# Performance work log

Hardware: AMD Instinct MI355X
Metric: run time of the kernel (lower is better)

## Reference

```python
import jax, jax.numpy as jnp
import numpy as np

OUT_SL = 32


def gru_cell(x, h, Wih, Whh, bih, bhh):
    # PyTorch GRU cell: gates ordered (r, z, n)
    gi = x @ Wih.T + bih
    gh = h @ Whh.T + bhh
    ir, iz, inn = jnp.split(gi, 3, axis=-1)
    hr, hz, hn = jnp.split(gh, 3, axis=-1)
    r = jax.nn.sigmoid(ir + hr)
    z = jax.nn.sigmoid(iz + hz)
    n = jnp.tanh(inn + r * hn)
    return (1.0 - z) * n + z * h


def run_gru_layer(xs, h0, Wih, Whh, bih, bhh, reverse=False):
    def step(h, x):
        h = gru_cell(x, h, Wih, Whh, bih, bhh)
        return h, h
    hT, ys = jax.lax.scan(step, h0, xs, reverse=reverse)
    return ys, hT


def setup_inputs() -> dict:
    key = jax.random.key(0)
    ks = iter(jax.random.split(key, 32))

    def p(shape, fan_in):
        return (jax.random.normal(next(ks), shape, dtype=jnp.float32)
                / np.sqrt(fan_in).astype(np.float32))

    V_ENC, V_DEC, EE, ED, NH = 32000, 32000, 300, 300, 256
    inp = jax.random.randint(next(ks), (128, 64), 0, V_ENC)
    return {
        'emb_enc': p((V_ENC, EE), 1.0),
        'enc_Wih0': p((2, 3 * NH, EE), EE),
        'enc_Whh0': p((2, 3 * NH, NH), NH),
        'enc_bih0': p((2, 3 * NH), NH),
        'enc_bhh0': p((2, 3 * NH), NH),
        'enc_Wih1': p((2, 3 * NH, 2 * NH), 2 * NH),
        'enc_Whh1': p((2, 3 * NH, NH), NH),
        'enc_bih1': p((2, 3 * NH), NH),
        'enc_bhh1': p((2, 3 * NH), NH),
        'W_out_enc': p((ED, 2 * NH), 2 * NH),
        'emb_dec': p((V_DEC, ED), 1.0),
        'dec_Wih': p((2, 3 * ED, ED), ED),
        'dec_Whh': p((2, 3 * ED, ED), ED),
        'dec_bih': p((2, 3 * ED), ED),
        'dec_bhh': p((2, 3 * ED), ED),
        'W1': p((2 * NH, ED), 2 * NH),
        'l2_W': p((ED, ED), ED),
        'l2_b': p((ED,), ED),
        'l3_W': p((ED, ED + 2 * NH), ED + 2 * NH),
        'l3_b': p((ED,), ED),
        'V_att': p((ED,), ED),
        'out_b': p((V_DEC,), ED),
        'inp': inp,
    }


def reference(emb_enc, enc_Wih0, enc_Whh0, enc_bih0, enc_bhh0,
              enc_Wih1, enc_Whh1, enc_bih1, enc_bhh1, W_out_enc,
              emb_dec, dec_Wih, dec_Whh, dec_bih, dec_bhh,
              W1, l2_W, l2_b, l3_W, l3_b, V_att, out_b, inp):
    sl, bs = inp.shape
    nh = enc_Whh0.shape[-1]
    h0 = jnp.zeros((bs, nh), dtype=emb_enc.dtype)

    # ---- encoder: 2-layer bidirectional GRU (dropout in eval mode = identity)
    emb = emb_enc[inp]                                        # (sl, bs, EE)
    yf0, hf0 = run_gru_layer(emb, h0, enc_Wih0[0], enc_Whh0[0], enc_bih0[0], enc_bhh0[0])
    yb0, hb0 = run_gru_layer(emb, h0, enc_Wih0[1], enc_Whh0[1], enc_bih0[1], enc_bhh0[1], reverse=True)
    x1 = jnp.concatenate([yf0, yb0], axis=-1)                 # (sl, bs, 2*nh)
    yf1, hf1 = run_gru_layer(x1, h0, enc_Wih1[0], enc_Whh1[0], enc_bih1[0], enc_bhh1[0])
    yb1, hb1 = run_gru_layer(x1, h0, enc_Wih1[1], enc_Whh1[1], enc_bih1[1], enc_bhh1[1], reverse=True)
    enc_out = jnp.concatenate([yf1, yb1], axis=-1)            # (sl, bs, 2*nh)

    # h.view(2,2,bs,-1).permute(0,2,1,3) -> concat fwd/bwd per layer
    h = jnp.stack([jnp.concatenate([hf0, hb0], axis=-1),
                   jnp.concatenate([hf1, hb1], axis=-1)])     # (2, bs, 2*nh)
    h = h @ W_out_enc.T                                       # (2, bs, ED)

    w1e = enc_out @ W1                                        # (sl, bs, ED)
    dec_inp0 = jnp.zeros((bs,), dtype=jnp.int32)

    def dec_step(carry, _):
        h, dec_inp = carry
        w2h = h[-1] @ l2_W.T + l2_b                           # (bs, ED)
        u = jnp.tanh(w1e + w2h[None])                         # (sl, bs, ED)
        a = jax.nn.softmax(u @ V_att, axis=0)                 # (sl, bs), softmax over seq
        Xa = jnp.einsum('sb,sbd->bd', a, enc_out)             # (bs, 2*nh)
        e = emb_dec[dec_inp]                                  # (bs, ED)
        x = jnp.concatenate([e, Xa], axis=1) @ l3_W.T + l3_b  # (bs, ED)
        h0n = gru_cell(x, h[0], dec_Wih[0], dec_Whh[0], dec_bih[0], dec_bhh[0])
        h1n = gru_cell(h0n, h[1], dec_Wih[1], dec_Whh[1], dec_bih[1], dec_bhh[1])
        outp = h1n @ emb_dec.T + out_b                        # (bs, V_dec), tied weights
        ndec = jnp.argmax(outp, axis=1).astype(jnp.int32)
        return (jnp.stack([h0n, h1n]), ndec), outp

    (_, _), res = jax.lax.scan(dec_step, (h, dec_inp0), None, length=OUT_SL)
    return res                                                # (out_sl, bs, V_dec)
```

## Files before the change

kernel.cpp:

```cpp
#include <hip/hip_runtime.h>
#include <math.h>


typedef unsigned long long ull;
typedef float v2f __attribute__((ext_vector_type(2)));

#define DINL static __device__ __forceinline__

DINL float sigm(float x) { return 1.0f / (1.0f + expf(-x)); }
DINL float dot4f(float4 a, float4 b) { return a.x*b.x + a.y*b.y + a.z*b.z + a.w*b.w; }

DINL ull packmax(float x, int v) {
  unsigned u = __float_as_uint(x);
  u = (u & 0x80000000u) ? ~u : (u | 0x80000000u);
  return ((ull)u << 32) | (unsigned)(~v);
}
DINL ull umax64(ull a, ull b) { return a > b ? a : b; }

DINL float atl(const float* p) {
  unsigned u = __hip_atomic_load((const unsigned*)p, __ATOMIC_RELAXED,
                                 __HIP_MEMORY_SCOPE_AGENT);
  return __uint_as_float(u);
}
DINL void atsf(float* p, float v) {
  __hip_atomic_exchange((unsigned*)p, __float_as_uint(v), __ATOMIC_RELAXED,
                        __HIP_MEMORY_SCOPE_AGENT);
}
DINL ull atl64(const ull* p) {
  return __hip_atomic_load(p, __ATOMIC_RELAXED, __HIP_MEMORY_SCOPE_AGENT);
}
DINL void ats64(ull* p, ull v) {
  __hip_atomic_exchange(p, v, __ATOMIC_RELAXED, __HIP_MEMORY_SCOPE_AGENT);
}

DINL void gbar(unsigned* flags, int wg, unsigned target, int tid) {
  asm volatile("s_waitcnt vmcnt(0)" ::: "memory");
  __syncthreads();
  if (tid == 0)
    __hip_atomic_exchange(&flags[wg * 32], target, __ATOMIC_RELAXED,
                          __HIP_MEMORY_SCOPE_AGENT);
  while (__hip_atomic_load(&flags[tid * 32], __ATOMIC_RELAXED,
                           __HIP_MEMORY_SCOPE_AGENT) < target)
    __builtin_amdgcn_s_sleep(1);
  __syncthreads();
}

__global__ __launch_bounds__(256) void k_embed(const float4* __restrict__ E,
                                               const int* __restrict__ inp,
                                               float4* __restrict__ out) {
  int i = blockIdx.x * 256 + threadIdx.x;
  if (i >= 8192 * 75) return;
  int row = i / 75, q = i - row * 75;
  out[i] = E[(size_t)inp[row] * 75 + q];
}

__global__ __launch_bounds__(256) void k_transpose(const float* __restrict__ A,
                                                   float* __restrict__ B, int R, int C) {
  __shared__ float tile[32][33];
  int c0 = blockIdx.x * 32, r0 = blockIdx.y * 32;
  int tx = threadIdx.x & 31, ty = threadIdx.x >> 5;
  for (int i = 0; i < 32; i += 8) {
    int r = r0 + ty + i, c = c0 + tx;
    if (r < R && c < C) tile[ty + i][tx] = A[(size_t)r * C + c];
  }
  __syncthreads();
  for (int i = 0; i < 32; i += 8) {
    int c = c0 + ty + i, r = r0 + tx;
    if (c < C && r < R) B[(size_t)c * R + r] = tile[tx][ty + i];
  }
}

__global__ __launch_bounds__(256) void k_packW(const float* __restrict__ Whh,
                                               float* __restrict__ W2) {
  int i = blockIdx.x * 256 + threadIdx.x;
  if (i >= 196608) return;
  int d = i / 98304, r = i - d * 98304, kp = r / 768, gc = r - kp * 768;
  const float* src = Whh + (size_t)d * 196608 + (size_t)gc * 256 + kp * 2;
  float* dst = W2 + (size_t)i * 2;
  dst[0] = src[0];
  dst[1] = src[1];
}

__global__ __launch_bounds__(256) void k_gemm128(const float* __restrict__ A,
                                                 const float* __restrict__ B,
                                                 const float* __restrict__ bias,
                                                 float* __restrict__ C,
                                                 int N, int M, int K) {
  __shared__ float As[8][132];
  __shared__ float Bs[8][132];
  const int tid = threadIdx.x;
  const int bn = blockIdx.x * 128, bm = blockIdx.y * 128;
  const int tn = (tid >> 4) << 3, tm = (tid & 15) << 3;
  const int r = tid & 127;
  const bool isB = tid >= 128;
  const float* src = isB ? (B + (size_t)(bm + r) * K) : (A + (size_t)(bn + r) * K);
  const bool rowok = isB ? (bm + r < M) : (bn + r < N);
  float acc[8][8] = {};
  for (int k0 = 0; k0 < K; k0 += 8) {
    float v[8];
    if (rowok && k0 + 8 <= K) {
      float4 p0 = *(const float4*)(src + k0);
      float4 p1 = *(const float4*)(src + k0 + 4);
      v[0]=p0.x; v[1]=p0.y; v[2]=p0.z; v[3]=p0.w;
      v[4]=p1.x; v[5]=p1.y; v[6]=p1.z; v[7]=p1.w;
    } else {
#pragma unroll
      for (int j = 0; j < 8; ++j) v[j] = (rowok && k0 + j < K) ? src[k0 + j] : 0.0f;
    }
    float (*dst)[132] = isB ? Bs : As;
#pragma unroll
    for (int j = 0; j < 8; ++j) dst[j][r] = v[j];
    __syncthreads();
#pragma unroll
    for (int kk = 0; kk < 8; ++kk) {
      float a[8], b[8];
      *(float4*)&a[0] = *(const float4*)&As[kk][tn];
      *(float4*)&a[4] = *(const float4*)&As[kk][tn + 4];
      *(float4*)&b[0] = *(const float4*)&Bs[kk][tm];
      *(float4*)&b[4] = *(const float4*)&Bs[kk][tm + 4];
#pragma unroll
      for (int i = 0; i < 8; ++i)
#pragma unroll
        for (int j = 0; j < 8; ++j) acc[i][j] += a[i] * b[j];
    }
    __syncthreads();
  }
#pragma unroll
  for (int i = 0; i < 8; ++i) {
    int row = bn + tn + i;
    if (row >= N) continue;
#pragma unroll
    for (int j = 0; j < 8; ++j) {
      int col = bm + tm + j;
      if (col < M) C[(size_t)row * M + col] = acc[i][j] + (bias ? bias[col] : 0.0f);
    }
  }
}

__global__ __launch_bounds__(256) void k_enc_rec(
    const float* __restrict__ giF, const float* __restrict__ giB,
    const float* __restrict__ W2,
    const float* __restrict__ bhh,
    float* __restrict__ y) {
  const int b0 = blockIdx.x * 2;
  const int dir = blockIdx.y;
  const int c = threadIdx.x;
  const float* gi = dir ? giB : giF;
  const v2f* Wv = (const v2f*)(W2 + (size_t)dir * 196608);
  const float* bh = bhh + dir * 768;

  __shared__ __align__(16) float hls[2][2][258];
  for (int i = c; i < 2 * 2 * 258; i += 256) ((float*)hls)[i] = 0.0f;
  __syncthreads();

  const float bhr = bh[c], bhz = bh[256 + c], bhn = bh[512 + c];

  const int tt0 = dir ? 127 : 0;
  const float* g0p = gi + (size_t)tt0 * 49152 + (size_t)b0 * 768;
  float g0r = g0p[c], g0z = g0p[256 + c], g0n = g0p[512 + c];
  float g1r = g0p[768 + c], g1z = g0p[1024 + c], g1n = g0p[1280 + c];

  for (int t = 0; t < 128; ++t) {
    const int cu = t & 1;
    float p0r = 0, p0z = 0, p0n = 0, p1r = 0, p1z = 0, p1n = 0;
    if (t < 127) {
      const int tn_ = dir ? 126 - t : t + 1;
      const float* gp = gi + (size_t)tn_ * 49152 + (size_t)b0 * 768;
      p0r = gp[c]; p0z = gp[256 + c]; p0n = gp[512 + c];
      p1r = gp[768 + c]; p1z = gp[1024 + c]; p1n = gp[1280 + c];
    }
    v2f a0r = {0,0}, a0z = {0,0}, a0n = {0,0};
    v2f a1r = {0,0}, a1z = {0,0}, a1n = {0,0};
    const float* h0p = &hls[cu][0][0];
    const float* h1p = &hls[cu][1][0];
#pragma unroll 4
    for (int kp = 0; kp < 128; ++kp) {
      v2f wr = Wv[kp * 768 + c];
      v2f wz = Wv[kp * 768 + 256 + c];
      v2f wn = Wv[kp * 768 + 512 + c];
      v2f h0 = *(const v2f*)&h0p[kp * 2];
      v2f h1 = *(const v2f*)&h1p[kp * 2];
      a0r += h0 * wr; a0z += h0 * wz; a0n += h0 * wn;
      a1r += h1 * wr; a1z += h1 * wz; a1n += h1 * wn;
    }
    float r0 = sigm(g0r + a0r.x + a0r.y + bhr);
    float z0 = sigm(g0z + a0z.x + a0z.y + bhz);
    float n0 = tanhf(g0n + r0 * (a0n.x + a0n.y + bhn));
    float h0new = (1.f - z0) * n0 + z0 * h0p[c];
    float r1 = sigm(g1r + a1r.x + a1r.y + bhr);
    float z1 = sigm(g1z + a1z.x + a1z.y + bhz);
    float n1 = tanhf(g1n + r1 * (a1n.x + a1n.y + bhn));
    float h1new = (1.f - z1) * n1 + z1 * h1p[c];
    hls[cu ^ 1][0][c] = h0new;
    hls[cu ^ 1][1][c] = h1new;
    const int tw = dir ? 127 - t : t;
    float* yp = y + (size_t)tw * 32768 + (size_t)b0 * 512 + dir * 256 + c;
    yp[0] = h0new;
    yp[512] = h1new;
    g0r = p0r; g0z = p0z; g0n = p0n; g1r = p1r; g1z = p1z; g1n = p1n;
    __syncthreads();
  }
}

__global__ __launch_bounds__(256) void k_hcat(const float* __restrict__ x1,
                                              const float* __restrict__ encout,
                                              float* __restrict__ hcat) {
  int i = blockIdx.x * 256 + threadIdx.x;
  int l = i >> 15, r = i & 32767, b = r >> 9, d = r & 511;
  const float* src = l ? encout : x1;
  int ts = (d < 256) ? 127 : 0;
  hcat[i] = src[((size_t)(ts << 6) + b) * 512 + d];
}

DINL void gru_at(int cb, int tid, const float* __restrict__ xin,
                 const float* __restrict__ hin, float* __restrict__ hout,
                 float* __restrict__ houtT,
                 const float* __restrict__ Wih, const float* __restrict__ Whh,
                 const float* __restrict__ bih, const float* __restrict__ bhh,
                 float* xs, float* hs) {
  const int cchunk = cb % 19, bchunk = cb / 19;
  const int cl = tid & 15, bl = tid >> 4;
  const int c = cchunk * 16 + cl;
  const int b0 = bchunk * 16, bq = b0 + bl;
  for (int i = tid; i < 4800; i += 256) {
    int row = i / 300, q = i - row * 300;
    xs[i] = atl(xin + (size_t)(b0 + row) * 300 + q);
    hs[i] = atl(hin + (size_t)(b0 + row) * 300 + q);
  }
  __syncthreads();
  if (c < 300) {
    float gir = bih[c], giz = bih[300 + c], gin = bih[600 + c];
    float ghr = bhh[c], ghz = bhh[300 + c], ghn = bhh[600 + c];
    const float4* wir = (const float4*)(Wih + (size_t)c * 300);
    const float4* wiz = (const float4*)(Wih + (size_t)(300 + c) * 300);
    const float4* win = (const float4*)(Wih + (size_t)(600 + c) * 300);
    const float4* whr = (const float4*)(Whh + (size_t)c * 300);
    const float4* whz = (const float4*)(Whh + (size_t)(300 + c) * 300);
    const float4* whn = (const float4*)(Whh + (size_t)(600 + c) * 300);
    const float4* xr = (const float4*)(xs + bl * 300);
    const float4* hr = (const float4*)(hs + bl * 300);
    for (int q = 0; q < 75; ++q) {
      float4 xv = xr[q], hv = hr[q];
      gir += dot4f(xv, wir[q]);
      giz += dot4f(xv, wiz[q]);
      gin += dot4f(xv, win[q]);
      ghr += dot4f(hv, whr[q]);
      ghz += dot4f(hv, whz[q]);
      ghn += dot4f(hv, whn[q]);
    }
    float r = sigm(gir + ghr), z = sigm(giz + ghz);
    float n = tanhf(gin + r * ghn);
    float hnew = (1.f - z) * n + z * hs[bl * 300 + c];
    atsf(&hout[(size_t)bq * 300 + c], hnew);
    if (houtT) atsf(&houtT[(size_t)c * 64 + bq], hnew);
  }
}

__global__ __launch_bounds__(256) void k_dec_all(
    float* __restrict__ dech, float* __restrict__ h1T, float* __restrict__ xdec,
    ull* __restrict__ bests, unsigned* __restrict__ flags,
    const float* __restrict__ w1e, const float* __restrict__ encout,
    const float* __restrict__ l2W, const float* __restrict__ l2b,
    const float* __restrict__ l3W, const float* __restrict__ l3b,
    const float* __restrict__ Vatt, const float* __restrict__ embdec,
    const float* __restrict__ dWih, const float* __restrict__ dWhh,
    const float* __restrict__ dbih, const float* __restrict__ dbhh,
    const float* __restrict__ embT, const float* __restrict__ outb,
    float* __restrict__ out) {
  const int wg = blockIdx.x, tid = threadIdx.x;
  __shared__ __align__(16) float smem[14400];
  unsigned tgt = 0;

  for (int t = 0; t < 32; ++t) {
    const int cur = t & 1;
    float* hc = dech + cur * 38400;
    float* hn = dech + (cur ^ 1) * 38400;

    if (wg < 64) {
      const int b = wg;
      float* h1s = smem;
      float* w2h = smem + 304;
      float* eXa = smem + 608;
      float* aa  = smem + 1424;
      float* red = smem + 1552;
      ull* redb  = (ull*)(smem + 1680);

      redb[tid] = (t > 0 && tid < 250) ? atl64(&bests[(size_t)tid * 64 + b]) : 0ULL;
      for (int i = tid; i < 300; i += 256) h1s[i] = atl(hc + 19200 + b * 300 + i);
      __syncthreads();
      for (int s = 128; s > 0; s >>= 1) {
        if (tid < s) redb[tid] = umax64(redb[tid], redb[tid + s]);
        __syncthreads();
      }
      const int ib = (t > 0) ? (int)(~(unsigned)(redb[0] & 0xFFFFFFFFULL)) : 0;

      for (int m = tid; m < 300; m += 256) {
        const float4* wr = (const float4*)(l2W + (size_t)m * 300);
        const float4* hr = (const float4*)h1s;
        float acc = l2b[m];
        for (int q = 0; q < 75; ++q) acc += dot4f(wr[q], hr[q]);
        w2h[m] = acc;
      }
      __syncthreads();

      if (tid < 128) {
        const float4* wp = (const float4*)(w1e + ((size_t)(tid << 6) + b) * 300);
        const float4* vp = (const float4*)Vatt;
        const float4* hp = (const float4*)w2h;
        float acc = 0.f;
        for (int q = 0; q < 75; ++q) {
          float4 w = wp[q], h = hp[q], v = vp[q];
          acc += tanhf(w.x + h.x) * v.x + tanhf(w.y + h.y) * v.y +
                 tanhf(w.z + h.z) * v.z + tanhf(w.w + h.w) * v.w;
        }
        aa[tid] = acc;
        red[tid] = acc;
      }
      __syncthreads();
      for (int s = 64; s > 0; s >>= 1) {
        if (tid < s) red[tid] = fmaxf(red[tid], red[tid + s]);
        __syncthreads();
      }
      float mx = red[0];
      __syncthreads();
      if (tid < 128) {
        float ex = expf(aa[tid] - mx);
        aa[tid] = ex;
        red[tid] = ex;
      }
      __syncthreads();
      for (int s = 64; s > 0; s >>= 1) {
        if (tid < s) red[tid] += red[tid + s];
        __syncthreads();
      }
      float inv = 1.0f / red[0];
      __syncthreads();
      if (tid < 128) aa[tid] *= inv;
      for (int d = tid; d < 300; d += 256) eXa[d] = embdec[(size_t)ib * 300 + d];
      __syncthreads();

      for (int d = tid; d < 512; d += 256) {
        float acc = 0.f;
        for (int s = 0; s < 128; ++s)
          acc += aa[s] * encout[((size_t)(s << 6) + b) * 512 + d];
        eXa[300 + d] = acc;
      }
      __syncthreads();

      for (int m = tid; m < 300; m += 256) {
        const float4* wr = (const float4*)(l3W + (size_t)m * 812);
        const float4* xr = (const float4*)eXa;
        float acc = l3b[m];
        for (int q = 0; q < 203; ++q) acc += dot4f(wr[q], xr[q]);
        atsf(&xdec[b * 300 + m], acc);
      }
    }
    gbar(flags, wg, ++tgt, tid);

    if (wg < 76)
      gru_at(wg, tid, xdec, hc, hn, nullptr, dWih, dWhh, dbih, dbhh,
             smem, smem + 4800);
    gbar(flags, wg, ++tgt, tid);

    if (wg < 76)
      gru_at(wg, tid, hn, hc + 19200, hn + 19200, h1T,
             dWih + 270000, dWhh + 270000, dbih + 900, dbhh + 900,
             smem, smem + 4800);
    gbar(flags, wg, ++tgt, tid);

    if (wg < 250) {
      const int v0 = wg * 128;
      const int vq = tid & 31, bo = tid >> 5;
      float acc[8][4];
#pragma unroll
      for (int i = 0; i < 8; ++i)
#pragma unroll
        for (int j = 0; j < 4; ++j) acc[i][j] = 0.f;
      float* hch = smem;
      float* et  = smem + 4800;
      for (int kc = 0; kc < 4; ++kc) {
        __syncthreads();
        for (int i = tid; i < 4800; i += 256) hch[i] = atl(h1T + kc * 4800 + i);
        for (int i = tid; i < 2400; i += 256) {
          int row = i >> 5, c4 = (i & 31) << 2;
          *(float4*)&et[(row << 7) + c4] =
              *(const float4*)(embT + (size_t)(kc * 75 + row) * 32000 + v0 + c4);
        }
        __syncthreads();
        for (int k = 0; k < 75; ++k) {
          float hv[8];
          *(float4*)&hv[0] = *(const float4*)&hch[(k << 6) + (bo << 3)];
          *(float4*)&hv[4] = *(const float4*)&hch[(k << 6) + (bo << 3) + 4];
          float4 ev = *(const float4*)&et[(k << 7) + (vq << 2)];
#pragma unroll
          for (int i = 0; i < 8; ++i) {
            acc[i][0] += hv[i] * ev.x;
            acc[i][1] += hv[i] * ev.y;
            acc[i][2] += hv[i] * ev.z;
            acc[i][3] += hv[i] * ev.w;
          }
        }
      }
      float4 bo4 = *(const float4*)(outb + v0 + (vq << 2));
      float* outp = out + (size_t)t * 2048000;
      float* sacc = smem;
      __syncthreads();
#pragma unroll
      for (int i = 0; i < 8; ++i) {
        const int b = (bo << 3) + i;
        float4 r;
        r.x = acc[i][0] + bo4.x; r.y = acc[i][1] + bo4.y;
        r.z = acc[i][2] + bo4.z; r.w = acc[i][3] + bo4.w;
        *(float4*)(outp + (size_t)b * 32000 + v0 + (vq << 2)) = r;
        sacc[((vq << 2) + 0) * 64 + b] = r.x;
        sacc[((vq << 2) + 1) * 64 + b] = r.y;
        sacc[((vq << 2) + 2) * 64 + b] = r.z;
        sacc[((vq << 2) + 3) * 64 + b] = r.w;
      }
      __syncthreads();
      if (tid < 64) {
        ull best = 0ULL;
#pragma unroll 4
        for (int v = 0; v < 128; ++v)
          best = umax64(best, packmax(sacc[v * 64 + tid], v0 + v));
        ats64(&bests[(size_t)wg * 64 + tid], best);
      }
    }
    if (t < 31) gbar(flags, wg, ++tgt, tid);
  }
}

extern "C" void kernel_launch(void* const* d_in, const int* in_sizes, int n_in,
                              void* d_out_v, int out_size, void* d_ws, size_t ws_size,
                              hipStream_t stream) {
  (void)in_sizes; (void)n_in; (void)out_size; (void)ws_size;
  const float* emb_enc = (const float*)d_in[0];
  const float* eWih0   = (const float*)d_in[1];
  const float* eWhh0   = (const float*)d_in[2];
  const float* ebih0   = (const float*)d_in[3];
  const float* ebhh0   = (const float*)d_in[4];
  const float* eWih1   = (const float*)d_in[5];
  const float* eWhh1   = (const float*)d_in[6];
  const float* ebih1   = (const float*)d_in[7];
  const float* ebhh1   = (const float*)d_in[8];
  const float* Wout    = (const float*)d_in[9];
  const float* emb_dec = (const float*)d_in[10];
  const float* dWih    = (const float*)d_in[11];
  const float* dWhh    = (const float*)d_in[12];
  const float* dbih    = (const float*)d_in[13];
  const float* dbhh    = (const float*)d_in[14];
  const float* W1      = (const float*)d_in[15];
  const float* l2W     = (const float*)d_in[16];
  const float* l2b     = (const float*)d_in[17];
  const float* l3W     = (const float*)d_in[18];
  const float* l3b     = (const float*)d_in[19];
  const float* Vatt    = (const float*)d_in[20];
  const float* outb    = (const float*)d_in[21];
  const int* inp       = (const int*)d_in[22];
  float* d_out = (float*)d_out_v;

  float* ws = (float*)d_ws;
  size_t off = 0;
  auto take = [&](size_t n) { float* p = ws + off; off += (n + 3) & ~(size_t)3; return p; };
  float* embT   = take((size_t)300 * 32000);
  float* encout = take((size_t)8192 * 512);
  float* w1e    = take((size_t)8192 * 300);
  float* W1T    = take((size_t)300 * 512);
  float* hcat   = take((size_t)128 * 512);
  float* dech   = take((size_t)2 * 2 * 64 * 300);
  float* h1T    = take((size_t)300 * 64);
  float* xdec   = take((size_t)64 * 300);
  ull* bests    = (ull*)take((size_t)250 * 64 * 2);
  unsigned* flags = (unsigned*)take((size_t)256 * 32);

  float* emb  = d_out;
  float* gi0f = emb + 2457600;
  float* gi0b = gi0f + 6291456;
  float* x1   = gi0b + 6291456;
  float* gi1f = x1 + 4194304;
  float* gi1b = gi1f + 6291456;
  float* W2L0 = d_out + 33554432;
  float* W2L1 = W2L0 + 393216;

  hipMemsetAsync(flags, 0, 256 * 32 * sizeof(unsigned), stream);

  k_embed<<<2400, 256, 0, stream>>>((const float4*)emb_enc, inp, (float4*)emb);
  k_transpose<<<dim3(10, 16), 256, 0, stream>>>(W1, W1T, 512, 300);
  k_transpose<<<dim3(10, 1000), 256, 0, stream>>>(emb_dec, embT, 32000, 300);
  k_packW<<<768, 256, 0, stream>>>(eWhh0, W2L0);
  k_packW<<<768, 256, 0, stream>>>(eWhh1, W2L1);

  k_gemm128<<<dim3(64, 6), 256, 0, stream>>>(emb, eWih0, ebih0, gi0f, 8192, 768, 300);
  k_gemm128<<<dim3(64, 6), 256, 0, stream>>>(emb, eWih0 + 230400, ebih0 + 768, gi0b, 8192, 768, 300);
  k_enc_rec<<<dim3(32, 2), 256, 0, stream>>>(gi0f, gi0b, W2L0, ebhh0, x1);

  k_gemm128<<<dim3(64, 6), 256, 0, stream>>>(x1, eWih1, ebih1, gi1f, 8192, 768, 512);
  k_gemm128<<<dim3(64, 6), 256, 0, stream>>>(x1, eWih1 + 393216, ebih1 + 768, gi1b, 8192, 768, 512);
  k_enc_rec<<<dim3(32, 2), 256, 0, stream>>>(gi1f, gi1b, W2L1, ebhh1, encout);

  k_hcat<<<256, 256, 0, stream>>>(x1, encout, hcat);
  k_gemm128<<<dim3(1, 3), 256, 0, stream>>>(hcat, Wout, nullptr, dech, 128, 300, 512);
  k_gemm128<<<dim3(64, 3), 256, 0, stream>>>(encout, W1T, nullptr, w1e, 8192, 300, 512);

  k_dec_all<<<256, 256, 0, stream>>>(dech, h1T, xdec, bests, flags,
                                     w1e, encout, l2W, l2b, l3W, l3b,
                                     Vatt, emb_dec, dWih, dWhh, dbih, dbhh,
                                     embT, outb, d_out);
}
```

Baseline: 11.03 ms.

## Rework decoder persistent kernel: counter barrier, async LDS prefetch, split GRU layers

The per-workgroup flag barrier becomes a single atomic counter barrier, which cuts each barrier's polling from all 256 flags to one location but concentrates contention there. The output projection now loads the full h1T into LDS once and double-buffers embT tiles with global_load_lds, so the next tile's fetch overlaps the current FMA loop. Layer-2 GRU runs on a different set of workgroups (76-151), and the padded sacc stride reduces LDS bank conflicts. Assorted unroll pragmas, a shorter argmax reduction and a hoisted encoder-output address are added as well. The price is a larger shared-memory footprint, which can lower occupancy.

```diff
diff --git a/kernel.cpp b/kernel.cpp
--- a/kernel.cpp
+++ b/kernel.cpp
@@ -33,15 +33,20 @@
   __hip_atomic_exchange(p, v, __ATOMIC_RELAXED, __HIP_MEMORY_SCOPE_AGENT);
 }
 
-DINL void gbar(unsigned* flags, int wg, unsigned target, int tid) {
+DINL void gl_lds16(const float* gaddr, float* laddr) {
+  __builtin_amdgcn_global_load_lds(
+      (const __attribute__((address_space(1))) unsigned*)gaddr,
+      (__attribute__((address_space(3))) unsigned*)laddr, 16, 0, 0);
+}
+
+DINL void gbar(unsigned* cnt, unsigned target, int tid) {
   asm volatile("s_waitcnt vmcnt(0)" ::: "memory");
   __syncthreads();
-  if (tid == 0)
-    __hip_atomic_exchange(&flags[wg * 32], target, __ATOMIC_RELAXED,
-                          __HIP_MEMORY_SCOPE_AGENT);
-  while (__hip_atomic_load(&flags[tid * 32], __ATOMIC_RELAXED,
-                           __HIP_MEMORY_SCOPE_AGENT) < target)
-    __builtin_amdgcn_s_sleep(1);
+  if (tid == 0) {
+    __hip_atomic_fetch_add(cnt, 1u, __ATOMIC_RELAXED, __HIP_MEMORY_SCOPE_AGENT);
+    while (__hip_atomic_load(cnt, __ATOMIC_RELAXED, __HIP_MEMORY_SCOPE_AGENT) < target)
+      __builtin_amdgcn_s_sleep(4);
+  }
   __syncthreads();
 }
 
@@ -139,8 +144,7 @@
 
 __global__ __launch_bounds__(256) void k_enc_rec(
     const float* __restrict__ giF, const float* __restrict__ giB,
-    const float* __restrict__ W2,
-    const float* __restrict__ bhh,
+    const float* __restrict__ W2, const float* __restrict__ bhh,
     float* __restrict__ y) {
   const int b0 = blockIdx.x * 2;
   const int dir = blockIdx.y;
@@ -154,7 +158,6 @@
   __syncthreads();
 
   const float bhr = bh[c], bhz = bh[256 + c], bhn = bh[512 + c];
-
   const int tt0 = dir ? 127 : 0;
   const float* g0p = gi + (size_t)tt0 * 49152 + (size_t)b0 * 768;
   float g0r = g0p[c], g0z = g0p[256 + c], g0n = g0p[512 + c];
@@ -222,6 +225,7 @@
   const int cl = tid & 15, bl = tid >> 4;
   const int c = cchunk * 16 + cl;
   const int b0 = bchunk * 16, bq = b0 + bl;
+#pragma unroll 4
   for (int i = tid; i < 4800; i += 256) {
     int row = i / 300, q = i - row * 300;
     xs[i] = atl(xin + (size_t)(b0 + row) * 300 + q);
@@ -254,11 +258,12 @@
     atsf(&hout[(size_t)bq * 300 + c], hnew);
     if (houtT) atsf(&houtT[(size_t)c * 64 + bq], hnew);
   }
+  __syncthreads();
 }
 
 __global__ __launch_bounds__(256) void k_dec_all(
     float* __restrict__ dech, float* __restrict__ h1T, float* __restrict__ xdec,
-    ull* __restrict__ bests, unsigned* __restrict__ flags,
+    ull* __restrict__ bests, unsigned* __restrict__ cnt,
     const float* __restrict__ w1e, const float* __restrict__ encout,
     const float* __restrict__ l2W, const float* __restrict__ l2b,
     const float* __restrict__ l3W, const float* __restrict__ l3b,
@@ -268,13 +273,13 @@
     const float* __restrict__ embT, const float* __restrict__ outb,
     float* __restrict__ out) {
   const int wg = blockIdx.x, tid = threadIdx.x;
-  __shared__ __align__(16) float smem[14400];
+  __shared__ __align__(16) float smem[27392];
+
   unsigned tgt = 0;
-
   for (int t = 0; t < 32; ++t) {
-    const int cur = t & 1;
-    float* hc = dech + cur * 38400;
-    float* hn = dech + (cur ^ 1) * 38400;
+    const int cur_ = t & 1;
+    float* hc = dech + cur_ * 38400;
+    float* hn = dech + (cur_ ^ 1) * 38400;
 
     if (wg < 64) {
       const int b = wg;
@@ -285,10 +290,17 @@
       float* red = smem + 1552;
       ull* redb  = (ull*)(smem + 1680);
 
-      redb[tid] = (t > 0 && tid < 250) ? atl64(&bests[(size_t)tid * 64 + b]) : 0ULL;
+      if (tid < 128) {
+        ull m = 0ULL;
+        if (t > 0) {
+          m = atl64(&bests[(size_t)tid * 64 + b]);
+          if (tid + 128 < 250) m = umax64(m, atl64(&bests[(size_t)(tid + 128) * 64 + b]));
+        }
+        redb[tid] = m;
+      }
       for (int i = tid; i < 300; i += 256) h1s[i] = atl(hc + 19200 + b * 300 + i);
       __syncthreads();
-      for (int s = 128; s > 0; s >>= 1) {
+      for (int s = 64; s > 0; s >>= 1) {
         if (tid < s) redb[tid] = umax64(redb[tid], redb[tid + s]);
         __syncthreads();
       }
@@ -298,6 +310,7 @@
         const float4* wr = (const float4*)(l2W + (size_t)m * 300);
         const float4* hr = (const float4*)h1s;
         float acc = l2b[m];
+#pragma unroll 5
         for (int q = 0; q < 75; ++q) acc += dot4f(wr[q], hr[q]);
         w2h[m] = acc;
       }
@@ -308,6 +321,7 @@
         const float4* vp = (const float4*)Vatt;
         const float4* hp = (const float4*)w2h;
         float acc = 0.f;
+#pragma unroll 5
         for (int q = 0; q < 75; ++q) {
           float4 w = wp[q], h = hp[q], v = vp[q];
           acc += tanhf(w.x + h.x) * v.x + tanhf(w.y + h.y) * v.y +
@@ -340,9 +354,10 @@
       __syncthreads();
 
       for (int d = tid; d < 512; d += 256) {
+        const float* ebase = encout + (size_t)b * 512 + d;
         float acc = 0.f;
-        for (int s = 0; s < 128; ++s)
-          acc += aa[s] * encout[((size_t)(s << 6) + b) * 512 + d];
+#pragma unroll 8
+        for (int s = 0; s < 128; ++s) acc += aa[s] * ebase[(size_t)s * 32768];
         eXa[300 + d] = acc;
       }
       __syncthreads();
@@ -351,82 +366,118 @@
         const float4* wr = (const float4*)(l3W + (size_t)m * 812);
         const float4* xr = (const float4*)eXa;
         float acc = l3b[m];
+#pragma unroll 7
         for (int q = 0; q < 203; ++q) acc += dot4f(wr[q], xr[q]);
         atsf(&xdec[b * 300 + m], acc);
       }
-    }
-    gbar(flags, wg, ++tgt, tid);
+      __syncthreads();
+    }
+    gbar(cnt, 256u * (++tgt), tid);
 
     if (wg < 76)
       gru_at(wg, tid, xdec, hc, hn, nullptr, dWih, dWhh, dbih, dbhh,
              smem, smem + 4800);
-    gbar(flags, wg, ++tgt, tid);
-
-    if (wg < 76)
-      gru_at(wg, tid, hn, hc + 19200, hn + 19200, h1T,
+    gbar(cnt, 256u * (++tgt), tid);
+
+    if (wg >= 76 && wg < 152)
+      gru_at(wg - 76, tid, hn, hc + 19200, hn + 19200, h1T,
              dWih + 270000, dWhh + 270000, dbih + 900, dbhh + 900,
              smem, smem + 4800);
-    gbar(flags, wg, ++tgt, tid);
+    gbar(cnt, 256u * (++tgt), tid);
 
     if (wg < 250) {
       const int v0 = wg * 128;
       const int vq = tid & 31, bo = tid >> 5;
-      float acc[8][4];
-#pragma unroll
-      for (int i = 0; i < 8; ++i)
-#pragma unroll
-        for (int j = 0; j < 4; ++j) acc[i][j] = 0.f;
+      const int wave = tid >> 6, lane = tid & 63;
       float* hch = smem;
-      float* et  = smem + 4800;
-      for (int kc = 0; kc < 4; ++kc) {
-        __syncthreads();
-        for (int i = tid; i < 4800; i += 256) hch[i] = atl(h1T + kc * 4800 + i);
-        for (int i = tid; i < 2400; i += 256) {
-          int row = i >> 5, c4 = (i & 31) << 2;
-          *(float4*)&et[(row << 7) + c4] =
-              *(const float4*)(embT + (size_t)(kc * 75 + row) * 32000 + v0 + c4);
+      float* lb  = smem + 19200;
+
+#pragma unroll 8
+      for (int i = tid; i < 19200; i += 256) hch[i] = atl(h1T + i);
+      {
+        const float* gb = embT + v0;
+#pragma unroll
+        for (int j = 0; j < 4; ++j) {
+          const int p = wave * 4 + j;
+          const int row = p * 2 + (lane >> 5);
+          gl_lds16(gb + (size_t)row * 32000 + ((lane & 31) << 2), lb + p * 256);
         }
-        __syncthreads();
-        for (int k = 0; k < 75; ++k) {
-          float hv[8];
-          *(float4*)&hv[0] = *(const float4*)&hch[(k << 6) + (bo << 3)];
-          *(float4*)&hv[4] = *(const float4*)&hch[(k << 6) + (bo << 3) + 4];
-          float4 ev = *(const float4*)&et[(k << 7) + (vq << 2)];
-#pragma unroll
-          for (int i = 0; i < 8; ++i) {
-            acc[i][0] += hv[i] * ev.x;
-            acc[i][1] += hv[i] * ev.y;
-            acc[i][2] += hv[i] * ev.z;
-            acc[i][3] += hv[i] * ev.w;
+      }
+      asm volatile("s_waitcnt vmcnt(0)" ::: "memory");
+      __syncthreads();
+
+      float acc[8][4] = {};
+      int cur = 0;
+      for (int kc = 0; kc < 10; ++kc) {
+        const int k0 = kc << 5;
+        const int nrows = (kc < 9) ? 32 : 12;
+        if (kc < 9) {
+          const int nrN = (kc + 1 < 9) ? 32 : 12;
+          const float* gb = embT + (size_t)(k0 + 32) * 32000 + v0;
+          float* lbn = lb + ((cur ^ 1) << 12);
+#pragma unroll
+          for (int j = 0; j < 4; ++j) {
+            const int p = wave * 4 + j;
+            if (p * 2 < nrN) {
+              const int row = p * 2 + (lane >> 5);
+              gl_lds16(gb + (size_t)row * 32000 + ((lane & 31) << 2), lbn + p * 256);
+            }
           }
         }
-      }
-      float4 bo4 = *(const float4*)(outb + v0 + (vq << 2));
+        const float* eb = lb + (cur << 12);
+#pragma unroll 8
+        for (int k = 0; k < nrows; ++k) {
+          float4 ev = *(const float4*)&eb[(k << 7) + (vq << 2)];
+          float4 h0 = *(const float4*)&hch[((k0 + k) << 6) + (bo << 3)];
+          float4 h1 = *(const float4*)&hch[((k0 + k) << 6) + (bo << 3) + 4];
+          acc[0][0] += h0.x * ev.x; acc[0][1] += h0.x * ev.y;
+          acc[0][2] += h0.x * ev.z; acc[0][3] += h0.x * ev.w;
+          acc[1][0] += h0.y * ev.x; acc[1][1] += h0.y * ev.y;
+          acc[1][2] += h0.y * ev.z; acc[1][3] += h0.y * ev.w;
+          acc[2][0] += h0.z * ev.x; acc[2][1] += h0.z * ev.y;
+          acc[2][2] += h0.z * ev.z; acc[2][3] += h0.z * ev.w;
+          acc[3][0] += h0.w * ev.x; acc[3][1] += h0.w * ev.y;
+          acc[3][2] += h0.w * ev.z; acc[3][3] += h0.w * ev.w;
+          acc[4][0] += h1.x * ev.x; acc[4][1] += h1.x * ev.y;
+          acc[4][2] += h1.x * ev.z; acc[4][3] += h1.x * ev.w;
+          acc[5][0] += h1.y * ev.x; acc[5][1] += h1.y * ev.y;
+          acc[5][2] += h1.y * ev.z; acc[5][3] += h1.y * ev.w;
+          acc[6][0] += h1.z * ev.x; acc[6][1] += h1.z * ev.y;
+          acc[6][2] += h1.z * ev.z; acc[6][3] += h1.z * ev.w;
+          acc[7][0] += h1.w * ev.x; acc[7][1] += h1.w * ev.y;
+          acc[7][2] += h1.w * ev.z; acc[7][3] += h1.w * ev.w;
+        }
+        asm volatile("s_waitcnt vmcnt(0)" ::: "memory");
+        __syncthreads();
+        cur ^= 1;
+      }
+
+      float* sacc = smem;
+      float4 ob = *(const float4*)(outb + v0 + (vq << 2));
       float* outp = out + (size_t)t * 2048000;
-      float* sacc = smem;
-      __syncthreads();
 #pragma unroll
       for (int i = 0; i < 8; ++i) {
         const int b = (bo << 3) + i;
         float4 r;
-        r.x = acc[i][0] + bo4.x; r.y = acc[i][1] + bo4.y;
-        r.z = acc[i][2] + bo4.z; r.w = acc[i][3] + bo4.w;
+        r.x = acc[i][0] + ob.x; r.y = acc[i][1] + ob.y;
+        r.z = acc[i][2] + ob.z; r.w = acc[i][3] + ob.w;
         *(float4*)(outp + (size_t)b * 32000 + v0 + (vq << 2)) = r;
-        sacc[((vq << 2) + 0) * 64 + b] = r.x;
-        sacc[((vq << 2) + 1) * 64 + b] = r.y;
-        sacc[((vq << 2) + 2) * 64 + b] = r.z;
-        sacc[((vq << 2) + 3) * 64 + b] = r.w;
+        sacc[((vq << 2) + 0) * 65 + b] = r.x;
+        sacc[((vq << 2) + 1) * 65 + b] = r.y;
+        sacc[((vq << 2) + 2) * 65 + b] = r.z;
+        sacc[((vq << 2) + 3) * 65 + b] = r.w;
       }
       __syncthreads();
       if (tid < 64) {
         ull best = 0ULL;
 #pragma unroll 4
         for (int v = 0; v < 128; ++v)
-          best = umax64(best, packmax(sacc[v * 64 + tid], v0 + v));
+          best = umax64(best, packmax(sacc[v * 65 + tid], v0 + v));
         ats64(&bests[(size_t)wg * 64 + tid], best);
       }
-    }
-    if (t < 31) gbar(flags, wg, ++tgt, tid);
+      __syncthreads();
+    }
+    if (t < 31) gbar(cnt, 256u * (++tgt), tid);
   }
 }
 
@@ -471,7 +522,7 @@
   float* h1T    = take((size_t)300 * 64);
   float* xdec   = take((size_t)64 * 300);
   ull* bests    = (ull*)take((size_t)250 * 64 * 2);
-  unsigned* flags = (unsigned*)take((size_t)256 * 32);
+  unsigned* cnt = (unsigned*)take((size_t)32);
 
   float* emb  = d_out;
   float* gi0f = emb + 2457600;
@@ -482,7 +533,7 @@
   float* W2L0 = d_out + 33554432;
   float* W2L1 = W2L0 + 393216;
 
-  hipMemsetAsync(flags, 0, 256 * 32 * sizeof(unsigned), stream);
+  hipMemsetAsync(cnt, 0, 32 * sizeof(unsigned), stream);
 
   k_embed<<<2400, 256, 0, stream>>>((const float4*)emb_enc, inp, (float4*)emb);
   k_transpose<<<dim3(10, 16), 256, 0, stream>>>(W1, W1T, 512, 300);
@@ -502,7 +553,7 @@
   k_gemm128<<<dim3(1, 3), 256, 0, stream>>>(hcat, Wout, nullptr, dech, 128, 300, 512);
   k_gemm128<<<dim3(64, 3), 256, 0, stream>>>(encout, W1T, nullptr, w1e, 8192, 300, 512);
 
-  k_dec_all<<<256, 256, 0, stream>>>(dech, h1T, xdec, bests, flags,
+  k_dec_all<<<256, 256, 0, stream>>>(dech, h1T, xdec, bests, cnt,
                                      w1e, encout, l2W, l2b, l3W, l3b,
                                      Vatt, emb_dec, dWih, dWhh, dbih, dbhh,
                                      embT, outb, d_out);
```

After: 11.28 ms. 2.3% more time.
